# Performance work log

Hardware: AMD Instinct MI355X
Metric: run time of the kernel (lower is better)

The kernel has to match this reference:

```python
import jax, jax.numpy as jnp
import numpy as np

C = 512  # in/out channel

def _w(key, shape, scale=0.02):
    return jax.random.normal(key, shape, dtype=jnp.float32) * scale

def setup_inputs() -> dict:
    key = jax.random.key(0)
    ks = jax.random.split(key, 16)
    B, N = 64, 256
    inp = {
        "rois_features": jax.random.normal(ks[0], (B, N, C), dtype=jnp.float32),
        "rois": jax.random.uniform(ks[1], (B, N, 5), dtype=jnp.float32),  # all >=0 -> all ROIs valid
        "rois_st_graph": jax.random.uniform(ks[2], (B, N, N), dtype=jnp.float32),
        # similarity-embedding Linear weights (torch Linear: y = x @ W.T), shape (out,in)
        "Wse1": _w(ks[3], (C, C)),
        "Wse2": _w(ks[4], (C, C)),
        # GraphConvolution weights (in,out): out = adj @ (x @ W)
        "Wst1": _w(ks[5], (C, C)), "Wst2": _w(ks[6], (C, C)), "Wst3": _w(ks[7], (C, C)),
        "Wst1b": _w(ks[8], (C, C)), "Wst2b": _w(ks[9], (C, C)), "Wst3b": _w(ks[10], (C, C)),
        "Wsim1": _w(ks[11], (C, C)), "Wsim2": _w(ks[12], (C, C)), "Wsim3": _w(ks[13], (C, C)),
    }
    return inp

def reference(rois_features, rois, rois_st_graph,
              Wse1, Wse2, Wst1, Wst2, Wst3, Wst1b, Wst2b, Wst3b,
              Wsim1, Wsim2, Wsim3):
    # All ROIs are valid (rois[:,:,0] >= 0 by construction), so the ragged
    # per-sample loop reduces to a uniform per-sample pipeline -> vmap.
    def gc(x, a, W):  # GraphConvolution: adj @ (x @ W)
        return a @ (x @ W)

    def per_sample(f, adj):  # f: (N,C), adj: (N,N)
        adjT = adj.T
        # similarity graph: softmax over rows of (f W1^T)(f W2^T)^T
        S = jax.nn.softmax((f @ Wse1.T) @ (f @ Wse2.T).T, axis=1)
        # st_GCN with separate forward/backward adjacency branches
        h = jax.nn.relu(gc(f, adj, Wst1)) + jax.nn.relu(gc(f, adjT, Wst1b))
        h = jax.nn.relu(gc(h, adj, Wst2)) + jax.nn.relu(gc(h, adjT, Wst2b))
        st = jax.nn.relu(gc(h, adj, Wst3)) + jax.nn.relu(gc(h, adjT, Wst3b))
        # sim_GCN
        g = jax.nn.relu(gc(f, S, Wsim1))
        g = jax.nn.relu(gc(g, S, Wsim2))
        g = jax.nn.relu(gc(g, S, Wsim3))
        return st + g

    out = jax.vmap(per_sample)(rois_features, rois_st_graph)  # (B, N, C)
    return out
```

## Files before the change

kernel.cpp:

```cpp
#include <hip/hip_runtime.h>
#include <stdint.h>

#define DEVI __device__ __forceinline__

using bf16x8 = __attribute__((ext_vector_type(8))) __bf16;
using f32x4  = __attribute__((ext_vector_type(4))) float;

DEVI ushort f2bf(float f){
  uint32_t u = __float_as_uint(f);
  uint32_t r = u + 0x7fffu + ((u >> 16) & 1u);
  return (ushort)(r >> 16);
}
DEVI float bf2f(ushort h){ return __uint_as_float(((uint32_t)h) << 16); }

DEVI void async16(const ushort* g, ushort* l, int lbyte) {
  __builtin_amdgcn_global_load_lds(
      (const __attribute__((address_space(1))) uint32_t*)g,
      (__attribute__((address_space(3))) uint32_t*)((char*)l + lbyte),
      16, 0, 0);
}

struct Seg {
  const ushort* A; const ushort* B; const void* Src; const void* Src2; void* O;
  long long sA, sB, sS, sS2, sO;
  int lda, ldb, ldS, ldS2, ldc;
  int K, nbx, nbxy, flags;
  long long A2off, B2off;
};

__global__ __launch_bounds__(256, 2)
void mega(Seg s0, Seg s1, Seg s2, int n0s, int n01)
{
  extern __shared__ __align__(16) ushort lds[];
  int bid = blockIdx.x;
  const Seg& s = (bid < n0s) ? s0 : ((bid < n01) ? s1 : s2);
  if (bid >= n0s) bid -= (bid < n01) ? n0s : n01;

  const int t = threadIdx.x;
  const int lane = t & 63, wave = t >> 6;
  const int lr = lane & 15, lq = lane >> 4;
  const int lb0 = __builtin_amdgcn_readfirstlane((t & 192) * 16);

#define MFMA16(Aa, Bb) { _Pragma("unroll") for (int x = 0; x < 4; x++)           \
    _Pragma("unroll") for (int y = 0; y < 4; y++)                                \
      acc[x][y] = __builtin_amdgcn_mfma_f32_16x16x32_bf16(Aa[x], Bb[y], acc[x][y], 0, 0, 0); }

  if (s.flags & 128) {
    const int z    = (bid & 7) + ((bid >> 6) << 3);
    const int slab = (bid >> 3) & 7;
    const int n0   = slab * 64;

    ushort* Yt  = lds;
    ushort* stA = lds + 16896;
    ushort* stW = lds + 25088;

    const int r0 = t >> 2, c0 = (t & 3) * 8;

    const ushort* X  = s.A + (long long)z * s.sA;
    const ushort* Wf = s.B + (long long)n0 * 512;
    const ushort* G0 = (const ushort*)s.Src + (long long)z * s.sS;

    f32x4 acc[4][4] = {};
    uint pk[4][4][2];
    const int npass = (s.flags & 16) ? 2 : 1;

    for (int p = 0; p < npass; ++p) {
      const ushort* Wp = p ? (Wf + s.B2off) : Wf;
      const ushort* Gp = p ? (G0 + s.A2off) : G0;
      const ushort* pX = X  + (long long)r0 * 512 + c0;
      const ushort* pW = Wp + (long long)r0 * 512 + c0;

      for (int k0 = 0; k0 < 512; k0 += 32) {
        __syncthreads();
        #pragma unroll
        for (int i = 0; i < 4; i++)
          async16(pX + (long long)(64*i)*512 + k0, stA, i*4096 + lb0);
        async16(pW + k0, stW, lb0);
        __syncthreads();
        bf16x8 af[4], bw[4];
        #pragma unroll
        for (int x = 0; x < 4; x++)
          af[x] = *(const bf16x8*)&stA[(64*wave + x*16 + lr)*32 + lq*8];
        #pragma unroll
        for (int y = 0; y < 4; y++)
          bw[y] = *(const bf16x8*)&stW[(y*16 + lr)*32 + lq*8];
        MFMA16(af, bw);
      }
      __syncthreads();
      #pragma unroll
      for (int x = 0; x < 4; x++)
        #pragma unroll
        for (int y = 0; y < 4; y++) {
          const int col  = y*16 + lr;
          const int rowb = 64*wave + x*16 + lq*4;
          uint2 v;
          v.x = (uint)f2bf(acc[x][y][0]) | ((uint)f2bf(acc[x][y][1]) << 16);
          v.y = (uint)f2bf(acc[x][y][2]) | ((uint)f2bf(acc[x][y][3]) << 16);
          *(uint2*)&Yt[col*264 + rowb] = v;
          acc[x][y] = (f32x4){0.f, 0.f, 0.f, 0.f};
        }
      const ushort* pG = Gp + (long long)r0 * s.ldS + c0;
      for (int k0 = 0; k0 < 256; k0 += 32) {
        __syncthreads();
        #pragma unroll
        for (int i = 0; i < 4; i++)
          async16(pG + (long long)(64*i)*s.ldS + k0, stA, i*4096 + lb0);
        __syncthreads();
        bf16x8 af[4], bfr[4];
        #pragma unroll
        for (int x = 0; x < 4; x++)
          af[x] = *(const bf16x8*)&stA[(64*wave + x*16 + lr)*32 + lq*8];
        #pragma unroll
        for (int y = 0; y < 4; y++)
          bfr[y] = *(const bf16x8*)&Yt[(y*16 + lr)*264 + k0 + lq*8];
        MFMA16(af, bfr);
      }
      if (p == 0 && npass == 2) {
        #pragma unroll
        for (int x = 0; x < 4; x++)
          #pragma unroll
          for (int y = 0; y < 4; y++) {
            pk[x][y][0] = (uint)f2bf(fmaxf(acc[x][y][0],0.f)) | ((uint)f2bf(fmaxf(acc[x][y][1],0.f)) << 16);
            pk[x][y][1] = (uint)f2bf(fmaxf(acc[x][y][2],0.f)) | ((uint)f2bf(fmaxf(acc[x][y][3],0.f)) << 16);
            acc[x][y] = (f32x4){0.f, 0.f, 0.f, 0.f};
          }
      }
    }
    const int fl = s.flags;
    #pragma unroll
    for (int x = 0; x < 4; x++)
      #pragma unroll
      for (int y = 0; y < 4; y++) {
        const int col = n0 + y*16 + lr;
        #pragma unroll
        for (int r = 0; r < 4; r++) {
          const int row = 64*wave + x*16 + lq*4 + r;
          float v = fmaxf(acc[x][y][r], 0.f);
          if (fl & 16) v += bf2f((ushort)(pk[x][y][r >> 1] >> (16*(r & 1))));
          if (fl & 4)  v += bf2f(((const ushort*)s.Src2)[(long long)z*s.sS2 + (long long)row*s.ldS2 + col]);
          if (fl & 2)
            ((ushort*)s.O)[(long long)z*s.sO + (long long)row*s.ldc + col] = f2bf(v);
          else
            ((float*)s.O)[(long long)z*s.sO + (long long)row*s.ldc + col] = v;
        }
      }
    return;
  }

  if (s.flags & 64) {
    const int niter = s.K >> 5;
    const int z = bid >> 2, mb = bid & 3;
    const ushort* pa = s.A + (long long)z*s.sA + (long long)(mb*64 + (t >> 2))*s.lda + (t & 3)*8;
    const ushort* pb = s.B + (long long)z*s.sB + (long long)(t >> 2)*s.ldb + (t & 3)*8;
    const long long b64 = 64ll*s.ldb;

    f32x4 acc[16] = {};
#define ISSUE_S(idx) { const int _i=(idx); const int _o=(_i&1)*20480 + lb0;      \
    const int _k=_i<<5;                                                          \
    async16(pa + _k, lds, _o);                                                   \
    async16(pb + _k,        lds, _o + 4096);                                     \
    async16(pb + b64 + _k,  lds, _o + 8192);                                     \
    async16(pb + 2*b64 + _k,lds, _o + 12288);                                    \
    async16(pb + 3*b64 + _k,lds, _o + 16384); }
    ISSUE_S(0);
    for (int i = 0; i < niter; ++i) {
      __syncthreads();
      if (i + 1 < niter) ISSUE_S(i + 1);
      const ushort* LA = lds + (i & 1)*10240;
      const ushort* LB = LA + 2048;
      const bf16x8 af = *(const bf16x8*)&LA[(wave*16 + lr)*32 + lq*8];
      #pragma unroll
      for (int j = 0; j < 16; j++) {
        const bf16x8 bfr = *(const bf16x8*)&LB[(j*16 + lr)*32 + lq*8];
        acc[j] = __builtin_amdgcn_mfma_f32_16x16x32_bf16(af, bfr, acc[j], 0, 0, 0);
      }
    }
    float mx[4] = {-1e30f, -1e30f, -1e30f, -1e30f};
    #pragma unroll
    for (int j = 0; j < 16; j++)
      #pragma unroll
      for (int r = 0; r < 4; r++) mx[r] = fmaxf(mx[r], acc[j][r]);
    #pragma unroll
    for (int r = 0; r < 4; r++)
      #pragma unroll
      for (int off = 1; off <= 8; off <<= 1) mx[r] = fmaxf(mx[r], __shfl_xor(mx[r], off, 64));
    float sm[4] = {0.f, 0.f, 0.f, 0.f};
    #pragma unroll
    for (int j = 0; j < 16; j++)
      #pragma unroll
      for (int r = 0; r < 4; r++) { float e = __expf(acc[j][r] - mx[r]); acc[j][r] = e; sm[r] += e; }
    #pragma unroll
    for (int r = 0; r < 4; r++) {
      #pragma unroll
      for (int off = 1; off <= 8; off <<= 1) sm[r] += __shfl_xor(sm[r], off, 64);
      sm[r] = 1.0f / sm[r];
    }
    ushort* Oz = (ushort*)s.O + (long long)z*s.sO;
    #pragma unroll
    for (int j = 0; j < 16; j++)
      #pragma unroll
      for (int r = 0; r < 4; r++) {
        const int row = mb*64 + wave*16 + lq*4 + r;
        Oz[(long long)row*s.ldc + j*16 + lr] = f2bf(acc[j][r]*sm[r]);
      }
    return;
  }

  {
    ushort* lA = lds;
    ushort* lB = lds + 4096;
    const int z  = bid / s.nbxy;
    const int rz = bid % s.nbxy;
    const int bx = rz % s.nbx, by = rz / s.nbx;
    const int wm = (wave >> 1)*64, wn = (wave & 1)*64;
    const int r0 = t >> 2, c0 = (t & 3)*8;

    const ushort* pa = s.A + (long long)z*s.sA + (long long)(by*128 + r0)*s.lda + c0;
    const ushort* pb = s.B + (long long)z*s.sB + (long long)(bx*128 + r0)*s.ldb + c0;
    const long long a64 = 64ll*s.lda, b64 = 64ll*s.ldb;

    f32x4 acc[4][4] = {};
    for (int k0 = 0; k0 < s.K; k0 += 32) {
      __syncthreads();
      async16(pa + k0,       lA, lb0);
      async16(pa + a64 + k0, lA, lb0 + 4096);
      async16(pb + k0,       lB, lb0);
      async16(pb + b64 + k0, lB, lb0 + 4096);
      __syncthreads();
      bf16x8 af[4], bfr[4];
      #pragma unroll
      for (int x = 0; x < 4; x++) {
        af[x]  = *(const bf16x8*)&lA[(wm + x*16 + lr)*32 + lq*8];
        bfr[x] = *(const bf16x8*)&lB[(wn + x*16 + lr)*32 + lq*8];
      }
      MFMA16(af, bfr);
    }
    const int rowb = by*128 + wm + lq*4;
    const int colb = bx*128 + wn + lr;
    const int fl = s.flags;
    #pragma unroll
    for (int x = 0; x < 4; x++)
      #pragma unroll
      for (int y = 0; y < 4; y++) {
        const int col = colb + y*16;
        #pragma unroll
        for (int r = 0; r < 4; r++) {
          const int row = rowb + x*16 + r;
          float v = acc[x][y][r];
          if (fl & 1) v = fmaxf(v, 0.f);
          if (fl & 2)
            ((ushort*)s.O)[(long long)z*s.sO + (long long)row*s.ldc + col] = f2bf(v);
          else
            ((float*)s.O)[(long long)z*s.sO + (long long)row*s.ldc + col] = v;
        }
      }
  }
}

struct P11 { const float* p[11]; };

__global__ void prep(const float* __restrict__ F, ushort* __restrict__ FB,
                     P11 ps, ushort* __restrict__ WT,
                     const float* __restrict__ ADJ, ushort* __restrict__ AB,
                     ushort* __restrict__ ATB)
{
  __shared__ float tile[32][33];
  const int b = blockIdx.x, t = threadIdx.x;
  if (b < 8192) {
    const int i = b*256 + t;
    const float4 v = ((const float4*)F)[i];
    ushort4 o; o.x = f2bf(v.x); o.y = f2bf(v.y); o.z = f2bf(v.z); o.w = f2bf(v.w);
    ((ushort4*)FB)[i] = o;
  } else if (b < 11008) {
    const int q = b - 8192;
    const int wdx = q >> 8, tl = q & 255;
    const int bo = (tl & 15)*32, bk = (tl >> 4)*32;
    const int tx = t & 31, ty = t >> 5;
    const float* in = ps.p[wdx];
    ushort* o = WT + (long long)wdx*262144;
    #pragma unroll
    for (int r = 0; r < 32; r += 8) tile[ty+r][tx] = in[(long long)(bk+ty+r)*512 + bo+tx];
    __syncthreads();
    #pragma unroll
    for (int r = 0; r < 32; r += 8) o[(long long)(bo+ty+r)*512 + bk+tx] = f2bf(tile[tx][ty+r]);
  } else {
    const int q = b - 11008;
    const long long base = (long long)(q >> 6)*65536;
    const int bi = ((q >> 3) & 7)*32, bj = (q & 7)*32;
    const int tx = t & 31, ty = t >> 5;
    #pragma unroll
    for (int r = 0; r < 32; r += 8) {
      const float v = ADJ[base + (long long)(bi+ty+r)*256 + bj+tx];
      tile[ty+r][tx] = v;
      AB[base + (long long)(bi+ty+r)*256 + bj+tx] = f2bf(v);
    }
    __syncthreads();
    #pragma unroll
    for (int r = 0; r < 32; r += 8)
      ATB[base + (long long)(bj+ty+r)*256 + bi+tx] = f2bf(tile[tx][ty+r]);
  }
}

extern "C" void kernel_launch(void* const* d_in, const int* in_sizes, int n_in,
                              void* d_out, int out_size, void* d_ws, size_t ws_size,
                              hipStream_t stream)
{
  (void)in_sizes; (void)n_in; (void)out_size;
  const float* F   = (const float*)d_in[0];
  const float* ADJ = (const float*)d_in[2];

  uint8_t* w = (uint8_t*)d_ws;
  size_t off = 0;
  auto alloc = [&](size_t bytes) -> void* { void* p = w + off; off += (bytes + 255) & ~(size_t)255; return p; };

  const long long SL = 262144;
  ushort* WT   = (ushort*)alloc(11*524288);
  ushort* WMT  = (ushort*)alloc(524288);
  ushort* FB   = (ushort*)alloc(16777216);
  ushort* ADJB = (ushort*)alloc(8388608);
  ushort* ADJT = (ushort*)alloc(8388608);
  ushort* TB   = (ushort*)alloc(16777216);
  ushort* Sb   = (ushort*)alloc(8388608);
  ushort* Hb   = (ushort*)alloc(16777216);
  ushort* Hb2  = (ushort*)alloc(16777216);
  ushort* Gb   = (ushort*)alloc(16777216);
  ushort* Gb2  = (ushort*)alloc(16777216);
  if (off > ws_size) return;

  const long long sNC = 131072, sNN = 65536;
  const int LDSB = 54272;

  auto zero = [](Seg& s) {
    s.A = nullptr; s.B = nullptr; s.Src = nullptr; s.Src2 = nullptr; s.O = nullptr;
    s.sA = s.sB = s.sS = s.sS2 = s.sO = 0;
    s.lda = s.ldb = s.ldS = s.ldS2 = s.ldc = 0;
    s.K = 0; s.nbx = 1; s.nbxy = 1; s.flags = 0; s.A2off = s.B2off = 0;
  };
  auto mkP = [&](const void* A, long long sA, int lda, const void* B, long long sB, int ldb,
                 void* O, long long sO, int ldc, int K, int M, int Nn, int flags) -> Seg {
    Seg s; zero(s);
    s.A = (const ushort*)A; s.B = (const ushort*)B; s.O = O;
    s.sA = sA; s.sB = sB; s.sO = sO;
    s.lda = lda; s.ldb = ldb; s.ldc = ldc;
    s.K = K; s.nbx = Nn/128; s.nbxy = (Nn/128)*(M/128); s.flags = flags;
    return s;
  };
  auto mkF = [&](const void* X, const void* Wf, long long B2off, const void* G, long long A2off,
                 const void* Src2, void* O, int flags) -> Seg {
    Seg s; zero(s);
    s.A = (const ushort*)X; s.sA = sNC; s.lda = 512;
    s.B = (const ushort*)Wf; s.B2off = B2off;
    s.Src = G; s.sS = sNN; s.ldS = 256; s.A2off = A2off;
    s.Src2 = Src2; s.sS2 = sNC; s.ldS2 = 512;
    s.O = O; s.sO = sNC; s.ldc = 512;
    s.flags = 128 | flags;
    return s;
  };
  auto L1 = [&](const Seg& a, int na) { mega<<<na, 256, LDSB, stream>>>(a, a, a, na, na); };
  auto L2 = [&](const Seg& a, int na, const Seg& b, int nb) {
    mega<<<na+nb, 256, LDSB, stream>>>(a, b, b, na, na+nb); };

  P11 ps;
  ps.p[0] = (const float*)d_in[5];  ps.p[1] = (const float*)d_in[8];
  ps.p[2] = (const float*)d_in[6];  ps.p[3] = (const float*)d_in[9];
  ps.p[4] = (const float*)d_in[7];  ps.p[5] = (const float*)d_in[10];
  ps.p[6] = (const float*)d_in[11]; ps.p[7] = (const float*)d_in[12];
  ps.p[8] = (const float*)d_in[13];
  ps.p[9] = (const float*)d_in[3];  ps.p[10] = (const float*)d_in[4];
  prep<<<15104, 256, 0, stream>>>(F, FB, ps, WT, ADJ, ADJB, ADJT);

  const long long dA = (long long)(ADJT - ADJB);

  Seg Wmid = mkP(WT+10*SL,0,512, WT+9*SL,0,512, WMT,0,512, 512, 512,512, 2);
  Seg Tsg  = mkP(FB,sNC,512, WMT,0,512, TB,sNC,512, 512, 256,512, 2);
  Seg ScS; zero(ScS);
  ScS.A = TB; ScS.B = FB; ScS.O = Sb;
  ScS.sA = sNC; ScS.sB = sNC; ScS.sO = sNN;
  ScS.lda = 512; ScS.ldb = 512; ScS.ldc = 256;
  ScS.K = 512; ScS.flags = 64;

  Seg ST1  = mkF(FB,  WT+0*SL, SL, ADJB, dA, nullptr, Hb,  16|2);
  Seg ST2  = mkF(Hb,  WT+2*SL, SL, ADJB, dA, nullptr, Hb2, 16|2);
  Seg ST3  = mkF(Hb2, WT+4*SL, SL, ADJB, dA, nullptr, Hb,  16|2);
  Seg SIM1 = mkF(FB,  WT+6*SL, 0,  Sb,   0,  nullptr, Gb,  2);
  Seg SIM2 = mkF(Gb,  WT+7*SL, 0,  Sb,   0,  nullptr, Gb2, 2);
  Seg SIM3 = mkF(Gb2, WT+8*SL, 0,  Sb,   0,  Hb,      d_out, 4);

  L2(Wmid,16, ST1,512);
  L2(Tsg,512, ST2,512);
  L2(ScS,256, ST3,512);
  L1(SIM1,512);
  L1(SIM2,512);
  L1(SIM3,512);
}
```

Baseline: 392.2 us.

## Double-buffer LDS tiles in GEMM and fused kernels with one barrier per step

Adds double-buffered LDS staging to all three K-loops: the fused X·W loop, the adjacency loop and the plain batched GEMM. The next tile's async global-to-LDS loads are issued right after the barrier, then the MFMAs run on the current buffer, which removes one barrier per iteration. The goal is to overlap global load latency with matrix work. LDS per block rises from 54272 to 74752 bytes, which can lower how many blocks fit on a CU.

```diff
diff --git a/kernel.cpp b/kernel.cpp
--- a/kernel.cpp
+++ b/kernel.cpp
@@ -50,9 +50,7 @@
     const int slab = (bid >> 3) & 7;
     const int n0   = slab * 64;
 
-    ushort* Yt  = lds;
-    ushort* stA = lds + 16896;
-    ushort* stW = lds + 25088;
+    ushort* Yt = lds;
 
     const int r0 = t >> 2, c0 = (t & 3) * 8;
 
@@ -70,23 +68,28 @@
       const ushort* pX = X  + (long long)r0 * 512 + c0;
       const ushort* pW = Wp + (long long)r0 * 512 + c0;
 
+#define ISSUE1(k0s, b) { const int _o = 33792 + (b)*20480 + lb0;                 \
+      _Pragma("unroll") for (int i = 0; i < 4; i++)                              \
+        async16(pX + (long long)(64*i)*512 + (k0s), lds, _o + i*4096);           \
+      async16(pW + (k0s), lds, _o + 16384); }
+
+      __syncthreads();
+      ISSUE1(0, 0);
       for (int k0 = 0; k0 < 512; k0 += 32) {
+        const int cur = (k0 >> 5) & 1;
         __syncthreads();
-        #pragma unroll
-        for (int i = 0; i < 4; i++)
-          async16(pX + (long long)(64*i)*512 + k0, stA, i*4096 + lb0);
-        async16(pW + k0, stW, lb0);
-        __syncthreads();
+        if (k0 + 32 < 512) ISSUE1(k0 + 32, cur ^ 1);
+        const ushort* sA = (const ushort*)((const char*)lds + 33792 + cur*20480);
+        const ushort* sW = sA + 8192;
         bf16x8 af[4], bw[4];
         #pragma unroll
         for (int x = 0; x < 4; x++)
-          af[x] = *(const bf16x8*)&stA[(64*wave + x*16 + lr)*32 + lq*8];
+          af[x] = *(const bf16x8*)&sA[(64*wave + x*16 + lr)*32 + lq*8];
         #pragma unroll
         for (int y = 0; y < 4; y++)
-          bw[y] = *(const bf16x8*)&stW[(y*16 + lr)*32 + lq*8];
+          bw[y] = *(const bf16x8*)&sW[(y*16 + lr)*32 + lq*8];
         MFMA16(af, bw);
       }
-      __syncthreads();
       #pragma unroll
       for (int x = 0; x < 4; x++)
         #pragma unroll
@@ -100,16 +103,22 @@
           acc[x][y] = (f32x4){0.f, 0.f, 0.f, 0.f};
         }
       const ushort* pG = Gp + (long long)r0 * s.ldS + c0;
+
+#define ISSUE2(k0s, b) { const int _o = 33792 + (b)*20480 + lb0;                 \
+      _Pragma("unroll") for (int i = 0; i < 4; i++)                              \
+        async16(pG + (long long)(64*i)*s.ldS + (k0s), lds, _o + i*4096); }
+
+      __syncthreads();
+      ISSUE2(0, 0);
       for (int k0 = 0; k0 < 256; k0 += 32) {
+        const int cur = (k0 >> 5) & 1;
         __syncthreads();
-        #pragma unroll
-        for (int i = 0; i < 4; i++)
-          async16(pG + (long long)(64*i)*s.ldS + k0, stA, i*4096 + lb0);
-        __syncthreads();
+        if (k0 + 32 < 256) ISSUE2(k0 + 32, cur ^ 1);
+        const ushort* sA = (const ushort*)((const char*)lds + 33792 + cur*20480);
         bf16x8 af[4], bfr[4];
         #pragma unroll
         for (int x = 0; x < 4; x++)
-          af[x] = *(const bf16x8*)&stA[(64*wave + x*16 + lr)*32 + lq*8];
+          af[x] = *(const bf16x8*)&sA[(64*wave + x*16 + lr)*32 + lq*8];
         #pragma unroll
         for (int y = 0; y < 4; y++)
           bfr[y] = *(const bf16x8*)&Yt[(y*16 + lr)*264 + k0 + lq*8];
@@ -207,8 +216,6 @@
   }
 
   {
-    ushort* lA = lds;
-    ushort* lB = lds + 4096;
     const int z  = bid / s.nbxy;
     const int rz = bid % s.nbxy;
     const int bx = rz % s.nbx, by = rz / s.nbx;
@@ -219,14 +226,20 @@
     const ushort* pb = s.B + (long long)z*s.sB + (long long)(bx*128 + r0)*s.ldb + c0;
     const long long a64 = 64ll*s.lda, b64 = 64ll*s.ldb;
 
+#define ISSUEP(k0s, b) { const int _o = (b)*16384 + lb0;                         \
+      async16(pa + (k0s),       lds, _o);                                        \
+      async16(pa + a64 + (k0s), lds, _o + 4096);                                 \
+      async16(pb + (k0s),       lds, _o + 8192);                                 \
+      async16(pb + b64 + (k0s), lds, _o + 12288); }
+
     f32x4 acc[4][4] = {};
+    ISSUEP(0, 0);
     for (int k0 = 0; k0 < s.K; k0 += 32) {
+      const int cur = (k0 >> 5) & 1;
       __syncthreads();
-      async16(pa + k0,       lA, lb0);
-      async16(pa + a64 + k0, lA, lb0 + 4096);
-      async16(pb + k0,       lB, lb0);
-      async16(pb + b64 + k0, lB, lb0 + 4096);
-      __syncthreads();
+      if (k0 + 32 < s.K) ISSUEP(k0 + 32, cur ^ 1);
+      const ushort* lA = (const ushort*)((const char*)lds + cur*16384);
+      const ushort* lB = lA + 4096;
       bf16x8 af[4], bfr[4];
       #pragma unroll
       for (int x = 0; x < 4; x++) {
@@ -328,7 +341,7 @@
   if (off > ws_size) return;
 
   const long long sNC = 131072, sNN = 65536;
-  const int LDSB = 54272;
+  const int LDSB = 74752;
 
   auto zero = [](Seg& s) {
     s.A = nullptr; s.B = nullptr; s.Src = nullptr; s.Src2 = nullptr; s.O = nullptr;
```

After: 417.4 us. 6.4% more time.

## Load MFMA operands directly from global memory, dropping LDS staging and barriers

Applied to the files above, without the earlier changes.

The fused GCN kernel and the generic batched GEMM path now read A/B fragments straight from global memory into registers, with an unrolled k-loop, instead of staging through LDS with async loads and two barriers per k-step. This removes synchronisation overhead and lets the compiler overlap loads with MFMAs. LDS is only kept for the Yt intermediate, so the dynamic LDS size shrinks, which may raise occupancy. The cost is that operands once shared across waves via LDS are now re-fetched per wave from cache, adding global/L2 traffic. Per-lane 16-byte loads with row strides may also coalesce less well.

```diff
diff --git a/kernel.cpp b/kernel.cpp
--- a/kernel.cpp
+++ b/kernel.cpp
@@ -50,11 +50,7 @@
     const int slab = (bid >> 3) & 7;
     const int n0   = slab * 64;
 
-    ushort* Yt  = lds;
-    ushort* stA = lds + 16896;
-    ushort* stW = lds + 25088;
-
-    const int r0 = t >> 2, c0 = (t & 3) * 8;
+    ushort* Yt = lds;
 
     const ushort* X  = s.A + (long long)z * s.sA;
     const ushort* Wf = s.B + (long long)n0 * 512;
@@ -64,27 +60,24 @@
     uint pk[4][4][2];
     const int npass = (s.flags & 16) ? 2 : 1;
 
+    const int arow = 64*wave + lr;
+
     for (int p = 0; p < npass; ++p) {
       const ushort* Wp = p ? (Wf + s.B2off) : Wf;
       const ushort* Gp = p ? (G0 + s.A2off) : G0;
-      const ushort* pX = X  + (long long)r0 * 512 + c0;
-      const ushort* pW = Wp + (long long)r0 * 512 + c0;
-
-      for (int k0 = 0; k0 < 512; k0 += 32) {
-        __syncthreads();
-        #pragma unroll
-        for (int i = 0; i < 4; i++)
-          async16(pX + (long long)(64*i)*512 + k0, stA, i*4096 + lb0);
-        async16(pW + k0, stW, lb0);
-        __syncthreads();
-        bf16x8 af[4], bw[4];
-        #pragma unroll
-        for (int x = 0; x < 4; x++)
-          af[x] = *(const bf16x8*)&stA[(64*wave + x*16 + lr)*32 + lq*8];
-        #pragma unroll
-        for (int y = 0; y < 4; y++)
-          bw[y] = *(const bf16x8*)&stW[(y*16 + lr)*32 + lq*8];
-        MFMA16(af, bw);
+
+      {
+        const ushort* pX = X  + (long long)arow * 512 + lq*8;
+        const ushort* pW = Wp + (long long)lr   * 512 + lq*8;
+        #pragma unroll 4
+        for (int k0 = 0; k0 < 512; k0 += 32) {
+          bf16x8 af[4], bw[4];
+          #pragma unroll
+          for (int x = 0; x < 4; x++) af[x] = *(const bf16x8*)(pX + x*8192 + k0);
+          #pragma unroll
+          for (int y = 0; y < 4; y++) bw[y] = *(const bf16x8*)(pW + y*8192 + k0);
+          MFMA16(af, bw);
+        }
       }
       __syncthreads();
       #pragma unroll
@@ -99,21 +92,18 @@
           *(uint2*)&Yt[col*264 + rowb] = v;
           acc[x][y] = (f32x4){0.f, 0.f, 0.f, 0.f};
         }
-      const ushort* pG = Gp + (long long)r0 * s.ldS + c0;
-      for (int k0 = 0; k0 < 256; k0 += 32) {
-        __syncthreads();
-        #pragma unroll
-        for (int i = 0; i < 4; i++)
-          async16(pG + (long long)(64*i)*s.ldS + k0, stA, i*4096 + lb0);
-        __syncthreads();
-        bf16x8 af[4], bfr[4];
-        #pragma unroll
-        for (int x = 0; x < 4; x++)
-          af[x] = *(const bf16x8*)&stA[(64*wave + x*16 + lr)*32 + lq*8];
-        #pragma unroll
-        for (int y = 0; y < 4; y++)
-          bfr[y] = *(const bf16x8*)&Yt[(y*16 + lr)*264 + k0 + lq*8];
-        MFMA16(af, bfr);
+      __syncthreads();
+      {
+        const ushort* pG = Gp + (long long)arow * 256 + lq*8;
+        #pragma unroll 4
+        for (int k0 = 0; k0 < 256; k0 += 32) {
+          bf16x8 af[4], bfr[4];
+          #pragma unroll
+          for (int x = 0; x < 4; x++) af[x] = *(const bf16x8*)(pG + x*4096 + k0);
+          #pragma unroll
+          for (int y = 0; y < 4; y++) bfr[y] = *(const bf16x8*)&Yt[(y*16 + lr)*264 + k0 + lq*8];
+          MFMA16(af, bfr);
+        }
       }
       if (p == 0 && npass == 2) {
         #pragma unroll
@@ -207,31 +197,23 @@
   }
 
   {
-    ushort* lA = lds;
-    ushort* lB = lds + 4096;
     const int z  = bid / s.nbxy;
     const int rz = bid % s.nbxy;
     const int bx = rz % s.nbx, by = rz / s.nbx;
     const int wm = (wave >> 1)*64, wn = (wave & 1)*64;
-    const int r0 = t >> 2, c0 = (t & 3)*8;
-
-    const ushort* pa = s.A + (long long)z*s.sA + (long long)(by*128 + r0)*s.lda + c0;
-    const ushort* pb = s.B + (long long)z*s.sB + (long long)(bx*128 + r0)*s.ldb + c0;
-    const long long a64 = 64ll*s.lda, b64 = 64ll*s.ldb;
+
+    const ushort* pA = s.A + (long long)z*s.sA + (long long)(by*128 + wm + lr)*s.lda + lq*8;
+    const ushort* pB = s.B + (long long)z*s.sB + (long long)(bx*128 + wn + lr)*s.ldb + lq*8;
+    const long long a16 = 16ll*s.lda, b16 = 16ll*s.ldb;
 
     f32x4 acc[4][4] = {};
+    #pragma unroll 4
     for (int k0 = 0; k0 < s.K; k0 += 32) {
-      __syncthreads();
-      async16(pa + k0,       lA, lb0);
-      async16(pa + a64 + k0, lA, lb0 + 4096);
-      async16(pb + k0,       lB, lb0);
-      async16(pb + b64 + k0, lB, lb0 + 4096);
-      __syncthreads();
       bf16x8 af[4], bfr[4];
       #pragma unroll
       for (int x = 0; x < 4; x++) {
-        af[x]  = *(const bf16x8*)&lA[(wm + x*16 + lr)*32 + lq*8];
-        bfr[x] = *(const bf16x8*)&lB[(wn + x*16 + lr)*32 + lq*8];
+        af[x]  = *(const bf16x8*)(pA + x*a16 + k0);
+        bfr[x] = *(const bf16x8*)(pB + x*b16 + k0);
       }
       MFMA16(af, bfr);
     }
@@ -328,7 +310,7 @@
   if (off > ws_size) return;
 
   const long long sNC = 131072, sNN = 65536;
-  const int LDSB = 54272;
+  const int LDSB = 40960;
 
   auto zero = [](Seg& s) {
     s.A = nullptr; s.B = nullptr; s.Src = nullptr; s.Src2 = nullptr; s.O = nullptr;
```

Result: slower. 587.0 us (+49.7%).
